# Performance work log

Hardware: AMD Instinct MI355X
Metric: run time of the kernel (lower is better)

The kernel has to match this reference:

```python
import jax, jax.numpy as jnp
import numpy as np

B, C, L, H, D = 2, 1024, 2048, 16, 64  # batch, n_factor, seq, heads, head_dim
LN_EPS = 1e-5


def setup_inputs() -> dict:
    key = jax.random.key(0)
    ks = jax.random.split(key, 8)
    s = 0.02
    return {
        "x": jax.random.normal(ks[0], (B, C, L), jnp.float32),
        "y": jax.random.normal(ks[1], (B, C, L), jnp.float32),
        "Wq": jax.random.normal(ks[2], (H, C, D), jnp.float32) * s,
        "Wk": jax.random.normal(ks[3], (H, C, D), jnp.float32) * s,
        "Wv": jax.random.normal(ks[4], (H, C, D), jnp.float32) * s,
        "bq": jax.random.normal(ks[5], (H, D), jnp.float32) * s,
        "bk": jax.random.normal(ks[6], (H, D), jnp.float32) * s,
        "bv": jax.random.normal(ks[7], (H, D), jnp.float32) * s,
        "gamma": jnp.ones((C,), jnp.float32),
        "beta": jnp.zeros((C,), jnp.float32),
    }


def reference(x, y, Wq, Wk, Wv, bq, bk, bv, gamma, beta):
    # Per-head Conv1d(kernel=1) == per-position linear; batch all heads at once.
    # x,y: [B, C, L]; W*: [H, C, D]; result q/k/v: [B, H, L, D]
    q = jnp.einsum('bcl,hcd->bhld', x, Wq) + bq[None, :, None, :]
    k = jnp.einsum('bcl,hcd->bhld', y, Wk) + bk[None, :, None, :]
    v = jnp.einsum('bcl,hcd->bhld', y, Wv) + bv[None, :, None, :]

    scale = 1.0 / jnp.sqrt(jnp.float32(D))  # n_factor_head ** 0.5
    scores = jnp.einsum('bhqd,bhkd->bhqk', q, k) * scale  # [B,H,L,L]
    attn = jax.nn.softmax(scores, axis=-1)
    ctx = jnp.einsum('bhqk,bhkd->bhqd', attn, v)  # [B,H,L,D]

    # torch.cat over heads along last dim == [B, L, H*D]
    att = jnp.transpose(ctx, (0, 2, 1, 3)).reshape(B, L, H * D)

    h = jnp.transpose(x, (0, 2, 1)) + att  # residual on x permuted to [B,L,C]
    mu = jnp.mean(h, axis=-1, keepdims=True)
    var = jnp.var(h, axis=-1, keepdims=True)
    out = (h - mu) * jax.lax.rsqrt(var + LN_EPS) * gamma + beta
    # dropout: identity in eval mode
    return out
```

## Files before the change

### kernel.cpp

```cpp
#include <hip/hip_runtime.h>
#include <hip/hip_bf16.h>

#define DEVI __device__ __forceinline__

typedef unsigned short u16;
typedef __bf16 bf16x8 __attribute__((ext_vector_type(8)));
typedef float f32x4 __attribute__((ext_vector_type(4)));

constexpr int Bn = 2, Cn = 1024, Ln = 2048, Hn = 16, Dn = 64;

DEVI u16 f2bfu(float f) { return __builtin_bit_cast(u16, __float2bfloat16(f)); }
DEVI float bfu2f(u16 u) { return __bfloat162float(__builtin_bit_cast(__hip_bfloat16, u)); }
DEVI f32x4 mfma16(bf16x8 a, bf16x8 b, f32x4 c) {
  return __builtin_amdgcn_mfma_f32_16x16x32_bf16(a, b, c, 0, 0, 0);
}
DEVI unsigned pk2(float lo, float hi) {
  return (unsigned)f2bfu(lo) | ((unsigned)f2bfu(hi) << 16);
}
DEVI void gld16(const u16* g, u16* l) {
  __builtin_amdgcn_global_load_lds(
      (const __attribute__((address_space(1))) unsigned*)g,
      (__attribute__((address_space(3))) unsigned*)l, 16, 0, 0);
}

__global__ __launch_bounds__(256) void transpose_xy(const float* __restrict__ x,
                                                    const float* __restrict__ y,
                                                    u16* __restrict__ xT,
                                                    u16* __restrict__ yT) {
  int z = blockIdx.z;
  int which = z >> 1, b = z & 1;
  const float* src = (which ? y : x) + (size_t)b * Cn * Ln;
  u16* dst = (which ? yT : xT) + (size_t)b * Ln * Cn;
  int l0 = blockIdx.x * 64, c0 = blockIdx.y * 64;
  __shared__ float tile[64][65];
  int t = threadIdx.x;
  #pragma unroll
  for (int i = 0; i < 16; ++i) {
    int idx = i * 256 + t;
    int r = idx >> 6, cc = idx & 63;
    tile[r][cc] = src[(size_t)(c0 + r) * Ln + (l0 + cc)];
  }
  __syncthreads();
  #pragma unroll
  for (int i = 0; i < 8; ++i) {
    int idx = i * 256 + t;
    int r = idx >> 5, cc = (idx & 31) * 2;
    unsigned pkv = pk2(tile[cc][r], tile[cc + 1][r]);
    *(unsigned*)(&dst[(size_t)(l0 + r) * Cn + (c0 + cc)]) = pkv;
  }
}

__global__ __launch_bounds__(256) void transpose_w(const float* __restrict__ Wq,
                                                   const float* __restrict__ Wk,
                                                   const float* __restrict__ Wv,
                                                   u16* __restrict__ WT) {
  int c0 = blockIdx.x * 64, h = blockIdx.y, which = blockIdx.z;
  const float* src = (which == 0 ? Wq : (which == 1 ? Wk : Wv)) + (size_t)h * Cn * Dn;
  u16* dst = WT + ((size_t)which * Hn + h) * Dn * Cn;
  __shared__ float tile[64][65];
  int t = threadIdx.x;
  #pragma unroll
  for (int i = 0; i < 16; ++i) {
    int idx = i * 256 + t;
    int r = idx >> 6, cc = idx & 63;
    tile[r][cc] = src[(size_t)(c0 + r) * Dn + cc];
  }
  __syncthreads();
  #pragma unroll
  for (int i = 0; i < 16; ++i) {
    int idx = i * 256 + t;
    int r = idx >> 6, cc = idx & 63;
    dst[(size_t)r * Cn + (c0 + cc)] = f2bfu(tile[cc][r]);
  }
}

__global__ __launch_bounds__(256) void gemm_qkv3(const u16* __restrict__ xT,
                                                 const u16* __restrict__ yT,
                                                 const u16* __restrict__ WT,
                                                 const float* __restrict__ bq,
                                                 const float* __restrict__ bk,
                                                 const float* __restrict__ bv,
                                                 u16* __restrict__ Qb,
                                                 u16* __restrict__ Kb,
                                                 u16* __restrict__ Vt) {
  int mt = blockIdx.x, by = blockIdx.y, b = blockIdx.z;
  int which = by >> 3, hp = by & 7;
  const u16* A = (which == 0 ? xT : yT) + (size_t)b * Ln * Cn + (size_t)mt * 128 * Cn;
  const u16* Bw = WT + ((size_t)which * 1024 + (size_t)hp * 128) * Cn;
  __shared__ __align__(16) u16 smem[2 * 128 * 64];
  u16* lA = smem;
  u16* lB = smem + 128 * 64;
  int t = threadIdx.x, wave = t >> 6, lane = t & 63;
  int wr = wave >> 1, wc = wave & 1;
  int ml = lane & 15, kg = lane >> 4;
  f32x4 acc[4][4] = {};
  for (int k0 = 0; k0 < Cn; k0 += 64) {
    __syncthreads();
    #pragma unroll
    for (int j = 0; j < 4; ++j) {
      int q = wave * 256 + j * 64 + lane;
      int row = q >> 3, p = q & 7, c16 = p ^ (row & 7);
      gld16(A + (size_t)row * Cn + k0 + c16 * 8, &lA[(wave * 256 + j * 64) * 8]);
    }
    #pragma unroll
    for (int j = 0; j < 4; ++j) {
      int q = wave * 256 + j * 64 + lane;
      int row = q >> 3, p = q & 7, c16 = p ^ (row & 7);
      gld16(Bw + (size_t)row * Cn + k0 + c16 * 8, &lB[(wave * 256 + j * 64) * 8]);
    }
    __syncthreads();
    bf16x8 af[4][2], bf[4][2];
    #pragma unroll
    for (int m = 0; m < 4; ++m) {
      int row = wr * 64 + m * 16 + ml;
      #pragma unroll
      for (int kk = 0; kk < 2; ++kk) {
        int p = (kk * 4 + kg) ^ (row & 7);
        af[m][kk] = *(const bf16x8*)(&lA[row * 64 + p * 8]);
      }
    }
    #pragma unroll
    for (int n = 0; n < 4; ++n) {
      int row = wc * 64 + n * 16 + ml;
      #pragma unroll
      for (int kk = 0; kk < 2; ++kk) {
        int p = (kk * 4 + kg) ^ (row & 7);
        bf[n][kk] = *(const bf16x8*)(&lB[row * 64 + p * 8]);
      }
    }
    #pragma unroll
    for (int m = 0; m < 4; ++m)
      #pragma unroll
      for (int n = 0; n < 4; ++n)
        #pragma unroll
        for (int kk = 0; kk < 2; ++kk)
          acc[m][n] = mfma16(af[m][kk], bf[n][kk], acc[m][n]);
  }
  int head = hp * 2 + wc;
  const float* bp = (which == 0 ? bq : (which == 1 ? bk : bv));
  if (which < 2) {
    u16* O = (which == 0 ? Qb : Kb) + (((size_t)b * Hn + head) * Ln + (size_t)mt * 128) * Dn;
    #pragma unroll
    for (int n = 0; n < 4; ++n) {
      float bvv = bp[head * 64 + n * 16 + ml];
      #pragma unroll
      for (int m = 0; m < 4; ++m)
        #pragma unroll
        for (int r = 0; r < 4; ++r) {
          int row = wr * 64 + m * 16 + kg * 4 + r;
          O[(size_t)row * Dn + n * 16 + ml] = f2bfu(acc[m][n][r] + bvv);
        }
    }
  } else {
    __syncthreads();
    #pragma unroll
    for (int n = 0; n < 4; ++n) {
      float bvv = bp[head * 64 + n * 16 + ml];
      int n_loc = wc * 64 + n * 16 + ml;
      int swz = (n_loc & 7) << 4;
      #pragma unroll
      for (int m = 0; m < 4; ++m) {
        int m_base = wr * 64 + m * 16 + kg * 4;
        uint2 pkd;
        pkd.x = pk2(acc[m][n][0] + bvv, acc[m][n][1] + bvv);
        pkd.y = pk2(acc[m][n][2] + bvv, acc[m][n][3] + bvv);
        *(uint2*)(&smem[n_loc * 128 + (m_base ^ swz)]) = pkd;
      }
    }
    __syncthreads();
    u16* Vbase = Vt + ((size_t)b * Hn + hp * 2) * Dn * Ln + (size_t)mt * 128;
    #pragma unroll
    for (int i = 0; i < 8; ++i) {
      int chunk = i * 256 + t;
      int n = chunk >> 4, cc = chunk & 15;
      uint4 vv = *(const uint4*)(&smem[n * 128 + (cc ^ ((n & 7) << 1)) * 8]);
      *(uint4*)(Vbase + (size_t)n * Ln + cc * 8) = vv;
    }
  }
}

__global__ __launch_bounds__(512, 8) void flash_attn(const u16* __restrict__ Qg,
                                                     const u16* __restrict__ Kg,
                                                     const u16* __restrict__ Vtg,
                                                     u16* __restrict__ att) {
  int qt = blockIdx.x, h = blockIdx.y, b = blockIdx.z;
  size_t bh = (size_t)b * Hn + h;
  const u16* Qp = Qg + (bh * Ln + (size_t)qt * 64) * Dn;
  const u16* Kp = Kg + bh * Ln * Dn;
  const u16* Vp = Vtg + bh * Dn * Ln;
  int t = threadIdx.x, wave = t >> 6, lane = t & 63;
  int qs = wave & 3, g = wave >> 2;
  int ml = lane & 15, kg = lane >> 4;
  __shared__ __align__(16) u16 Kl[2][64 * 64];
  __shared__ __align__(16) u16 Vl[2][64 * 64];
  __shared__ __align__(16) u16 Pl[8][16 * 32];
  u16* Pw = Pl[wave];

  constexpr float QS = 0.125f * 1.44269504f;
  bf16x8 qf[2];
  #pragma unroll
  for (int kk = 0; kk < 2; ++kk) {
    bf16x8 raw = *(const bf16x8*)(Qp + (size_t)(qs * 16 + ml) * Dn + kk * 32 + kg * 8);
    #pragma unroll
    for (int j = 0; j < 8; ++j) raw[j] = (__bf16)((float)raw[j] * QS);
    qf[kk] = raw;
  }

  f32x4 ctx[4] = {};
  float psum = 0.f;

  auto stage = [&](int buf, int kv0) {
    int rowk = t >> 3, p = t & 7, c16 = p ^ (rowk & 7);
    gld16(Kp + (size_t)(kv0 + rowk) * Dn + c16 * 8, &Kl[buf][wave * 512]);
    gld16(Vp + (size_t)rowk * Ln + kv0 + c16 * 8, &Vl[buf][wave * 512]);
  };

  stage(0, 0);
  __syncthreads();

  constexpr int NT = Ln / 64;
  for (int tt = 0; tt < NT; ++tt) {
    int cur = tt & 1;
    if (tt + 1 < NT) stage(cur ^ 1, (tt + 1) * 64);
    const u16* Kh = Kl[cur];
    const u16* Vh = Vl[cur];
    f32x4 s[2] = {};
    #pragma unroll
    for (int nt = 0; nt < 2; ++nt) {
      int row = g * 32 + nt * 16 + ml;
      #pragma unroll
      for (int kk = 0; kk < 2; ++kk) {
        int p = (kk * 4 + kg) ^ (row & 7);
        bf16x8 kf = *(const bf16x8*)(&Kh[row * 64 + p * 8]);
        s[nt] = mfma16(kf, qf[kk], s[nt]);
      }
    }
    #pragma unroll
    for (int nt = 0; nt < 2; ++nt) {
      f32x4 e;
      #pragma unroll
      for (int r = 0; r < 4; ++r) e[r] = __builtin_amdgcn_exp2f(s[nt][r]);
      psum += (e[0] + e[1]) + (e[2] + e[3]);
      uint2 pkd;
      pkd.x = pk2(e[0], e[1]);
      pkd.y = pk2(e[2], e[3]);
      int chunk = (nt * 2 + (kg >> 1)) ^ (ml & 3);
      *(uint2*)(&Pw[ml * 32 + chunk * 8 + (kg & 1) * 4]) = pkd;
    }
    bf16x8 pf = *(const bf16x8*)(&Pw[ml * 32 + (kg ^ (ml & 3)) * 8]);
    #pragma unroll
    for (int nt = 0; nt < 4; ++nt) {
      int row = nt * 16 + ml;
      int p = (g * 4 + kg) ^ (row & 7);
      bf16x8 vf = *(const bf16x8*)(&Vh[row * 64 + p * 8]);
      ctx[nt] = mfma16(pf, vf, ctx[nt]);
    }
    if (tt + 1 < NT) __syncthreads();
  }
  __syncthreads();
  float* comb = (float*)&Kl[0][0];
  float* psA = (float*)&Vl[0][0];
  if (g == 1) {
    int base = qs * 1024 + lane;
    #pragma unroll
    for (int nt = 0; nt < 4; ++nt)
      #pragma unroll
      for (int r = 0; r < 4; ++r)
        comb[base + (nt * 4 + r) * 64] = ctx[nt][r];
    psA[qs * 64 + lane] = psum;
  }
  __syncthreads();
  if (g == 0) {
    int base = qs * 1024 + lane;
    #pragma unroll
    for (int nt = 0; nt < 4; ++nt)
      #pragma unroll
      for (int r = 0; r < 4; ++r)
        ctx[nt][r] += comb[base + (nt * 4 + r) * 64];
    psum += psA[qs * 64 + lane];
    psum += __shfl_xor(psum, 16);
    psum += __shfl_xor(psum, 32);
    float inv[4];
    #pragma unroll
    for (int r = 0; r < 4; ++r) inv[r] = 1.f / __shfl(psum, kg * 4 + r);
    #pragma unroll
    for (int nt = 0; nt < 4; ++nt)
      #pragma unroll
      for (int r = 0; r < 4; ++r) {
        size_t row = (size_t)b * Ln + qt * 64 + qs * 16 + kg * 4 + r;
        att[row * Cn + h * Dn + nt * 16 + ml] = f2bfu(ctx[nt][r] * inv[r]);
      }
  }
}

__global__ __launch_bounds__(256) void ln_kernel(const u16* __restrict__ att,
                                                 const u16* __restrict__ xT,
                                                 const float* __restrict__ gamma,
                                                 const float* __restrict__ beta,
                                                 float* __restrict__ out) {
  size_t row = blockIdx.x;
  const u16* ap = att + row * Cn;
  const u16* xp = xT + row * Cn;
  float* op = out + row * Cn;
  int t = threadIdx.x;
  ushort4 a4 = *(const ushort4*)(ap + t * 4);
  ushort4 xv = *(const ushort4*)(xp + t * 4);
  float h0 = bfu2f(a4.x) + bfu2f(xv.x), h1 = bfu2f(a4.y) + bfu2f(xv.y);
  float h2 = bfu2f(a4.z) + bfu2f(xv.z), h3 = bfu2f(a4.w) + bfu2f(xv.w);
  float s = h0 + h1 + h2 + h3;
  float ss = h0 * h0 + h1 * h1 + h2 * h2 + h3 * h3;
  #pragma unroll
  for (int off = 1; off < 64; off <<= 1) {
    s += __shfl_xor(s, off);
    ss += __shfl_xor(ss, off);
  }
  __shared__ float red[8];
  int wave = t >> 6, lane = t & 63;
  if (lane == 0) { red[wave] = s; red[wave + 4] = ss; }
  __syncthreads();
  s = red[0] + red[1] + red[2] + red[3];
  ss = red[4] + red[5] + red[6] + red[7];
  float mu = s * (1.f / 1024.f);
  float var = ss * (1.f / 1024.f) - mu * mu;
  float rinv = rsqrtf(var + 1e-5f);
  float4 gmv = *(const float4*)(gamma + t * 4);
  float4 bev = *(const float4*)(beta + t * 4);
  float4 o;
  o.x = (h0 - mu) * rinv * gmv.x + bev.x;
  o.y = (h1 - mu) * rinv * gmv.y + bev.y;
  o.z = (h2 - mu) * rinv * gmv.z + bev.z;
  o.w = (h3 - mu) * rinv * gmv.w + bev.w;
  *(float4*)(op + t * 4) = o;
}

extern "C" void kernel_launch(void* const* d_in, const int* in_sizes, int n_in,
                              void* d_out, int out_size, void* d_ws, size_t ws_size,
                              hipStream_t stream) {
  const float* x = (const float*)d_in[0];
  const float* y = (const float*)d_in[1];
  const float* Wq = (const float*)d_in[2];
  const float* Wk = (const float*)d_in[3];
  const float* Wv = (const float*)d_in[4];
  const float* bq = (const float*)d_in[5];
  const float* bk = (const float*)d_in[6];
  const float* bv = (const float*)d_in[7];
  const float* gamma = (const float*)d_in[8];
  const float* beta = (const float*)d_in[9];
  float* out = (float*)d_out;

  char* ws = (char*)d_ws;
  u16* xT = (u16*)(ws + 0);
  u16* yT = (u16*)(ws + 8388608);
  u16* WT = (u16*)(ws + 16777216);
  u16* Qb = (u16*)(ws + 23068672);
  u16* Kb = (u16*)(ws + 31457280);
  u16* VT = (u16*)(ws + 39845888);
  u16* att = (u16*)(ws + 48234496);

  transpose_xy<<<dim3(Ln / 64, Cn / 64, 4), dim3(256), 0, stream>>>(x, y, xT, yT);
  transpose_w<<<dim3(Cn / 64, Hn, 3), dim3(256), 0, stream>>>(Wq, Wk, Wv, WT);
  gemm_qkv3<<<dim3(Ln / 128, 24, Bn), dim3(256), 0, stream>>>(xT, yT, WT, bq, bk, bv, Qb, Kb, VT);
  flash_attn<<<dim3(Ln / 64, Hn, Bn), dim3(512), 0, stream>>>(Qb, Kb, VT, att);
  ln_kernel<<<dim3(Bn * Ln), dim3(256), 0, stream>>>(att, xT, gamma, beta, out);
}
```

Baseline: 123.0 us.

## Keep softmax probabilities in registers by permuting K rows, remap blocks per XCD

The flash-attention kernel now permutes which K rows each lane loads, so the score MFMA output lands directly in the layout the P·V MFMA expects as its A operand. This removes the per-wave LDS round trip for P. It also changes the LDS swizzle to cut bank conflicts, adds s_setprio around the MFMA sections in both kernels, and remaps block IDs so blocks of the same head share an XCD for better L2 reuse of K and V. The risk is that the row permutation must stay consistent with the V layout, or the result is wrong.

```diff
diff --git a/kernel.cpp b/kernel.cpp
--- a/kernel.cpp
+++ b/kernel.cpp
@@ -22,6 +22,7 @@
       (const __attribute__((address_space(1))) unsigned*)g,
       (__attribute__((address_space(3))) unsigned*)l, 16, 0, 0);
 }
+DEVI int fsw(int row) { return (row & 7) ^ (((row >> 3) & 1) << 2); }
 
 __global__ __launch_bounds__(256) void transpose_xy(const float* __restrict__ x,
                                                     const float* __restrict__ y,
@@ -128,6 +129,7 @@
         bf[n][kk] = *(const bf16x8*)(&lB[row * 64 + p * 8]);
       }
     }
+    __builtin_amdgcn_s_setprio(1);
     #pragma unroll
     for (int m = 0; m < 4; ++m)
       #pragma unroll
@@ -135,6 +137,7 @@
         #pragma unroll
         for (int kk = 0; kk < 2; ++kk)
           acc[m][n] = mfma16(af[m][kk], bf[n][kk], acc[m][n]);
+    __builtin_amdgcn_s_setprio(0);
   }
   int head = hp * 2 + wc;
   const float* bp = (which == 0 ? bq : (which == 1 ? bk : bv));
@@ -183,7 +186,12 @@
                                                      const u16* __restrict__ Kg,
                                                      const u16* __restrict__ Vtg,
                                                      u16* __restrict__ att) {
-  int qt = blockIdx.x, h = blockIdx.y, b = blockIdx.z;
+  int n = blockIdx.x + 32 * (blockIdx.y + 16 * blockIdx.z);
+  int xcd = n & 7, m = n >> 3;
+  int grp = xcd * 4 + (m >> 5);
+  int qt = m & 31;
+  int h = grp & 15, b = grp >> 4;
+
   size_t bh = (size_t)b * Hn + h;
   const u16* Qp = Qg + (bh * Ln + (size_t)qt * 64) * Dn;
   const u16* Kp = Kg + bh * Ln * Dn;
@@ -193,8 +201,6 @@
   int ml = lane & 15, kg = lane >> 4;
   __shared__ __align__(16) u16 Kl[2][64 * 64];
   __shared__ __align__(16) u16 Vl[2][64 * 64];
-  __shared__ __align__(16) u16 Pl[8][16 * 32];
-  u16* Pw = Pl[wave];
 
   constexpr float QS = 0.125f * 1.44269504f;
   bf16x8 qf[2];
@@ -210,7 +216,7 @@
   float psum = 0.f;
 
   auto stage = [&](int buf, int kv0) {
-    int rowk = t >> 3, p = t & 7, c16 = p ^ (rowk & 7);
+    int rowk = t >> 3, p = t & 7, c16 = p ^ fsw(rowk);
     gld16(Kp + (size_t)(kv0 + rowk) * Dn + c16 * 8, &Kl[buf][wave * 512]);
     gld16(Vp + (size_t)rowk * Ln + kv0 + c16 * 8, &Vl[buf][wave * 512]);
   };
@@ -225,36 +231,39 @@
     const u16* Kh = Kl[cur];
     const u16* Vh = Vl[cur];
     f32x4 s[2] = {};
+    __builtin_amdgcn_s_setprio(1);
     #pragma unroll
     for (int nt = 0; nt < 2; ++nt) {
-      int row = g * 32 + nt * 16 + ml;
+      int rowk = g * 32 + 8 * (ml >> 2) + 4 * nt + (ml & 3);
       #pragma unroll
       for (int kk = 0; kk < 2; ++kk) {
-        int p = (kk * 4 + kg) ^ (row & 7);
-        bf16x8 kf = *(const bf16x8*)(&Kh[row * 64 + p * 8]);
+        int p = (kk * 4 + kg) ^ fsw(rowk);
+        bf16x8 kf = *(const bf16x8*)(&Kh[rowk * 64 + p * 8]);
         s[nt] = mfma16(kf, qf[kk], s[nt]);
       }
     }
-    #pragma unroll
-    for (int nt = 0; nt < 2; ++nt) {
-      f32x4 e;
-      #pragma unroll
-      for (int r = 0; r < 4; ++r) e[r] = __builtin_amdgcn_exp2f(s[nt][r]);
-      psum += (e[0] + e[1]) + (e[2] + e[3]);
-      uint2 pkd;
-      pkd.x = pk2(e[0], e[1]);
-      pkd.y = pk2(e[2], e[3]);
-      int chunk = (nt * 2 + (kg >> 1)) ^ (ml & 3);
-      *(uint2*)(&Pw[ml * 32 + chunk * 8 + (kg & 1) * 4]) = pkd;
-    }
-    bf16x8 pf = *(const bf16x8*)(&Pw[ml * 32 + (kg ^ (ml & 3)) * 8]);
+    __builtin_amdgcn_s_setprio(0);
+    f32x4 e0, e1;
+    #pragma unroll
+    for (int r = 0; r < 4; ++r) e0[r] = __builtin_amdgcn_exp2f(s[0][r]);
+    #pragma unroll
+    for (int r = 0; r < 4; ++r) e1[r] = __builtin_amdgcn_exp2f(s[1][r]);
+    psum += (e0[0] + e0[1]) + (e0[2] + e0[3]) + (e1[0] + e1[1]) + (e1[2] + e1[3]);
+    uint4 pw;
+    pw.x = pk2(e0[0], e0[1]);
+    pw.y = pk2(e0[2], e0[3]);
+    pw.z = pk2(e1[0], e1[1]);
+    pw.w = pk2(e1[2], e1[3]);
+    bf16x8 pf = __builtin_bit_cast(bf16x8, pw);
+    __builtin_amdgcn_s_setprio(1);
     #pragma unroll
     for (int nt = 0; nt < 4; ++nt) {
-      int row = nt * 16 + ml;
-      int p = (g * 4 + kg) ^ (row & 7);
-      bf16x8 vf = *(const bf16x8*)(&Vh[row * 64 + p * 8]);
+      int rowv = nt * 16 + ml;
+      int p = (g * 4 + kg) ^ fsw(rowv);
+      bf16x8 vf = *(const bf16x8*)(&Vh[rowv * 64 + p * 8]);
       ctx[nt] = mfma16(pf, vf, ctx[nt]);
     }
+    __builtin_amdgcn_s_setprio(0);
     if (tt + 1 < NT) __syncthreads();
   }
   __syncthreads();
```

New measurement: 109.8 us. 1.12x faster.
